# Performance work log

Measured on AMD Instinct MI355X. Metric: run time of the kernel, lower is better.

## Reference

```python
import jax, jax.numpy as jnp
import numpy as np

B, S, D = 4, 2048, 2048
H, G, HD = 16, 4, 128  # n_heads, kv groups, head_dim
EPS = 1e-6


def setup_inputs() -> dict:
    key = jax.random.key(0)
    ks = jax.random.split(key, 8)
    x = jax.random.normal(ks[0], (B, S, D), dtype=jnp.float32)
    # causal mask, True = attend (already 'inverted' for SDPA semantics)
    mask = jnp.tril(jnp.ones((S, S), dtype=bool))
    # RoPE tables: (S, HD), rotate-half convention with duplicated freqs
    inv_freq = 1.0 / (10000.0 ** (np.arange(0, HD, 2, dtype=np.float32) / HD))
    ang = np.arange(S, dtype=np.float32)[:, None] * inv_freq[None, :]  # (S, HD/2)
    ang = np.concatenate([ang, ang], axis=-1)  # (S, HD)
    cos = jnp.asarray(np.cos(ang))
    sin = jnp.asarray(np.sin(ang))
    s = 0.02
    wq = jax.random.normal(ks[1], (D, H * HD), dtype=jnp.float32) * s
    wk = jax.random.normal(ks[2], (D, G * HD), dtype=jnp.float32) * s
    wv = jax.random.normal(ks[3], (D, G * HD), dtype=jnp.float32) * s
    wg = jax.random.normal(ks[4], (D, H * HD), dtype=jnp.float32) * s
    wo = jax.random.normal(ks[5], (H * HD, D), dtype=jnp.float32) * s
    q_scale = jax.random.normal(ks[6], (HD,), dtype=jnp.float32) * 0.01  # zero-centered
    k_scale = jax.random.normal(ks[7], (HD,), dtype=jnp.float32) * 0.01
    return dict(x=x, mask=mask, cos=cos, sin=sin, wq=wq, wk=wk, wv=wv,
                wg=wg, wo=wo, q_scale=q_scale, k_scale=k_scale)


def _zc_rmsnorm(x, scale):
    # zero-centered RMSNorm in fp32: x * rsqrt(mean(x^2)+eps) * (1+scale)
    xf = x.astype(jnp.float32)
    rms = jax.lax.rsqrt(jnp.mean(xf * xf, axis=-1, keepdims=True) + EPS)
    return (xf * rms * (1.0 + scale)).astype(x.dtype)


def _rope(x, cos, sin):
    # x: (b, h, s, hd); cos/sin: (s, hd)
    hd = x.shape[-1]
    x1, x2 = x[..., : hd // 2], x[..., hd // 2 :]
    rot = jnp.concatenate([-x2, x1], axis=-1)
    return x * cos[None, None] + rot * sin[None, None]


def reference(x, mask, cos, sin, wq, wk, wv, wg, wo, q_scale, k_scale):
    b, s, d = x.shape
    q = (x @ wq).reshape(b, s, H, HD).transpose(0, 2, 1, 3)   # (b,H,s,hd)
    k = (x @ wk).reshape(b, s, G, HD).transpose(0, 2, 1, 3)   # (b,G,s,hd)
    v = (x @ wv).reshape(b, s, G, HD).transpose(0, 2, 1, 3)
    gate = jax.nn.sigmoid(x @ wg)                              # (b,s,H*HD)

    q = _rope(_zc_rmsnorm(q, q_scale), cos, sin)
    k = _rope(_zc_rmsnorm(k, k_scale), cos, sin)

    rep = H // G
    k = jnp.repeat(k, rep, axis=1)   # (b,H,s,hd)
    v = jnpep = jnp.repeat(v, rep, axis=1) if False else jnp.repeat(v, rep, axis=1)

    scores = jnp.einsum('bhqd,bhkd->bhqk', q, k) / jnp.sqrt(jnp.float32(HD))
    scores = jnp.where(mask[None, None, :s, :s], scores, jnp.float32(-1e30))
    attn = jax.nn.softmax(scores, axis=-1)
    ctx = jnp.einsum('bhqk,bhkd->bhqd', attn, v)               # (b,H,s,hd)
    ctx = ctx.transpose(0, 2, 1, 3).reshape(b, s, H * HD)
    return (ctx * gate) @ wo
```

## Files before the change

### kernel.cpp

```cpp
#include <hip/hip_runtime.h>

typedef __bf16 bf16;
typedef __attribute__((ext_vector_type(8))) __bf16 bf16x8;
typedef __attribute__((ext_vector_type(4))) float f32x4;

constexpr int Bb = 4, S = 2048, Dd = 2048, H = 16, G = 4, HD = 128;
constexpr float L2E = 1.4426950408889634f;

__device__ inline f32x4 mfma16(bf16x8 a, bf16x8 b, f32x4 c) {
  return __builtin_amdgcn_mfma_f32_16x16x32_bf16(a, b, c, 0, 0, 0);
}

__device__ inline void gl_lds16(const void* g, void* l) {
  __builtin_amdgcn_global_load_lds(
      (const __attribute__((address_space(1))) void*)g,
      (__attribute__((address_space(3))) void*)l, 16, 0, 0);
}

__global__ __launch_bounds__(256) void k_f32_to_bf16(
    const float* __restrict__ in, bf16* __restrict__ out, int n8) {
  int i = blockIdx.x * 256 + threadIdx.x;
  if (i >= n8) return;
  const float4* p = (const float4*)(in + (long long)i * 8);
  float4 a = p[0], b = p[1];
  bf16x8 v;
  v[0] = (bf16)a.x; v[1] = (bf16)a.y; v[2] = (bf16)a.z; v[3] = (bf16)a.w;
  v[4] = (bf16)b.x; v[5] = (bf16)b.y; v[6] = (bf16)b.z; v[7] = (bf16)b.w;
  *(bf16x8*)(out + (long long)i * 8) = v;
}

template <typename InT>
__global__ __launch_bounds__(256) void k_transpose_bf16(
    const InT* __restrict__ in, long long s1, int nb2, long long s2, int ldin,
    bf16* __restrict__ out, long long obatch, int ldout, int R, int C) {
  __shared__ float tile[32][33];
  int z = blockIdx.z;
  const InT* ip = in + (long long)(z / nb2) * s1 + (long long)(z % nb2) * s2;
  bf16* op = out + (long long)z * obatch;
  int c0 = blockIdx.x * 32, r0 = blockIdx.y * 32;
  int tx = threadIdx.x, ty = threadIdx.y;
#pragma unroll
  for (int i = 0; i < 4; ++i) {
    int r = r0 + ty + i * 8, c = c0 + tx;
    tile[ty + i * 8][tx] = (r < R && c < C) ? (float)ip[(long long)r * ldin + c] : 0.f;
  }
  __syncthreads();
#pragma unroll
  for (int i = 0; i < 4; ++i) {
    int c = c0 + ty + i * 8, r = r0 + tx;
    if (c < C && r < R) op[(long long)c * ldout + r] = (bf16)tile[tx][ty + i * 8];
  }
}

template <typename CT>
__global__ __launch_bounds__(512, 2) void k_gemm256(
    const bf16* __restrict__ A, int lda, const bf16* __restrict__ Bt, int ldb,
    CT* __restrict__ C, int ldc, int M, int N, int K) {
  __shared__ bf16 ldsbuf[65536];
  char* lds2 = (char*)ldsbuf;
  const int tid = threadIdx.x;
  const int w = tid >> 6, lane = tid & 63;
  const int l16 = lane & 15, lh = lane >> 4;
  const int wr = w >> 2, wc = w & 3;
  const int nbn = N >> 8;
  const int cpx = gridDim.x >> 3;
  const int swz = (blockIdx.x & 7) * cpx + (blockIdx.x >> 3);
  const int bm = swz / nbn, bn = swz % nbn;
  const int m0 = bm << 8, n0 = bn << 8;

  const int lrow = lane >> 3;
  const int lcol = ((lane & 7) ^ lrow) * 8;
  const int arb = wr * 128 + wc * 16;
  const int xg = wc >> 1, sg = wr * 2 + (wc & 1);
  const int brb = xg * 128 + (sg >> 1) * 64 + (sg & 1) * 16;
  const bf16* aS0 = A + (long long)(m0 + arb + lrow) * lda + lcol;
  const bf16* aS1 = A + (long long)(m0 + arb + 8 + lrow) * lda + lcol;
  const bf16* bS0 = Bt + (long long)(n0 + brb + lrow) * ldb + lcol;
  const bf16* bS1 = Bt + (long long)(n0 + brb + 8 + lrow) * ldb + lcol;

  auto stageA = [&](int buf, int k0, int hi) {
    gl_lds16(aS0 + (long long)hi * 64 * lda + k0,
             lds2 + buf * 65536 + (arb + hi * 64) * 128);
    gl_lds16(aS1 + (long long)hi * 64 * lda + k0,
             lds2 + buf * 65536 + (arb + hi * 64 + 8) * 128);
  };
  auto stageB = [&](int buf, int k0, int hi) {
    gl_lds16(bS0 + (long long)hi * 32 * ldb + k0,
             lds2 + buf * 65536 + 32768 + (brb + hi * 32) * 128);
    gl_lds16(bS1 + (long long)hi * 32 * ldb + k0,
             lds2 + buf * 65536 + 32768 + (brb + hi * 32 + 8) * 128);
  };

  f32x4 acc[8][4] = {};
  const int NT = K >> 6;

  stageA(0, 0, 0);
  stageB(0, 0, 0);
  stageB(0, 0, 1);
  stageA(0, 0, 1);
  asm volatile("s_waitcnt vmcnt(4)" ::: "memory");
  __builtin_amdgcn_s_barrier();

  const int swzc = (l16 & 7) << 4;
  for (int t = 0; t < NT; ++t) {
    const int buf = t & 1, nb = buf ^ 1;
    const int kn = (t + 1) << 6;
    const bool more = (t + 1 < NT);
    const char* La = lds2 + buf * 65536;
    const char* Lb = La + 32768;
    bf16x8 af[4][2], bn0[2][2], bn1[2][2];
    if (more) stageA(nb, kn, 0);
#pragma unroll
    for (int m = 0; m < 4; ++m)
#pragma unroll
      for (int ks = 0; ks < 2; ++ks)
        af[m][ks] = *(const bf16x8*)(La + (wr * 128 + m * 16 + l16) * 128 +
                                     ((ks * 64 + lh * 16) ^ swzc));
#pragma unroll
    for (int n = 0; n < 2; ++n)
#pragma unroll
      for (int ks = 0; ks < 2; ++ks)
        bn0[n][ks] = *(const bf16x8*)(Lb + (wc * 64 + n * 16 + l16) * 128 +
                                      ((ks * 64 + lh * 16) ^ swzc));
    __builtin_amdgcn_s_barrier();
    asm volatile("s_waitcnt lgkmcnt(0)" ::: "memory");
    __builtin_amdgcn_sched_barrier(0);
    __builtin_amdgcn_s_setprio(1);
#pragma unroll
    for (int m = 0; m < 4; ++m)
#pragma unroll
      for (int n = 0; n < 2; ++n)
#pragma unroll
        for (int ks = 0; ks < 2; ++ks)
          acc[m][n] = mfma16(af[m][ks], bn0[n][ks], acc[m][n]);
    __builtin_amdgcn_s_setprio(0);
    asm volatile("s_waitcnt vmcnt(4)" ::: "memory");
    __builtin_amdgcn_s_barrier();
    if (more) stageB(nb, kn, 0);
#pragma unroll
    for (int n = 0; n < 2; ++n)
#pragma unroll
      for (int ks = 0; ks < 2; ++ks)
        bn1[n][ks] = *(const bf16x8*)(Lb + (wc * 64 + 32 + n * 16 + l16) * 128 +
                                      ((ks * 64 + lh * 16) ^ swzc));
    __builtin_amdgcn_s_barrier();
    asm volatile("s_waitcnt lgkmcnt(0)" ::: "memory");
    __builtin_amdgcn_sched_barrier(0);
    __builtin_amdgcn_s_setprio(1);
#pragma unroll
    for (int m = 0; m < 4; ++m)
#pragma unroll
      for (int n = 0; n < 2; ++n)
#pragma unroll
        for (int ks = 0; ks < 2; ++ks)
          acc[m][2 + n] = mfma16(af[m][ks], bn1[n][ks], acc[m][2 + n]);
    __builtin_amdgcn_s_setprio(0);
    asm volatile("s_waitcnt vmcnt(4)" ::: "memory");
    __builtin_amdgcn_s_barrier();
    if (more) stageB(nb, kn, 1);
#pragma unroll
    for (int m = 0; m < 4; ++m)
#pragma unroll
      for (int ks = 0; ks < 2; ++ks)
        af[m][ks] = *(const bf16x8*)(La + (wr * 128 + 64 + m * 16 + l16) * 128 +
                                     ((ks * 64 + lh * 16) ^ swzc));
    __builtin_amdgcn_s_barrier();
    asm volatile("s_waitcnt lgkmcnt(0)" ::: "memory");
    __builtin_amdgcn_sched_barrier(0);
    __builtin_amdgcn_s_setprio(1);
#pragma unroll
    for (int m = 0; m < 4; ++m)
#pragma unroll
      for (int n = 0; n < 2; ++n)
#pragma unroll
        for (int ks = 0; ks < 2; ++ks)
          acc[4 + m][2 + n] = mfma16(af[m][ks], bn1[n][ks], acc[4 + m][2 + n]);
    __builtin_amdgcn_s_setprio(0);
    __builtin_amdgcn_s_barrier();
    if (more) stageA(nb, kn, 1);
    __builtin_amdgcn_s_barrier();
    __builtin_amdgcn_s_setprio(1);
#pragma unroll
    for (int m = 0; m < 4; ++m)
#pragma unroll
      for (int n = 0; n < 2; ++n)
#pragma unroll
        for (int ks = 0; ks < 2; ++ks)
          acc[4 + m][n] = mfma16(af[m][ks], bn0[n][ks], acc[4 + m][n]);
    __builtin_amdgcn_s_setprio(0);
    asm volatile("s_waitcnt vmcnt(4)" ::: "memory");
    __builtin_amdgcn_s_barrier();
  }

#pragma unroll
  for (int m = 0; m < 8; ++m)
#pragma unroll
    for (int n = 0; n < 4; ++n)
#pragma unroll
      for (int r = 0; r < 4; ++r)
        C[(long long)(m0 + wr * 128 + m * 16 + lh * 4 + r) * ldc + n0 + wc * 64 +
          n * 16 + l16] = (CT)acc[m][n][r];
}

__global__ __launch_bounds__(256) void k_rms_rope(
    const bf16* __restrict__ in, int ldin, int nh, const float* __restrict__ scale,
    const float* __restrict__ cosT, const float* __restrict__ sinT,
    bf16* __restrict__ out, float oscale, int nwaves) {
  int wid = (blockIdx.x * 256 + threadIdx.x) >> 6;
  if (wid >= nwaves) return;
  int lane = threadIdx.x & 63;
  int h = wid % nh;
  int bs = wid / nh;
  int s = bs % S;
  int b = bs / S;
  const bf16* ip = in + (long long)bs * ldin + h * HD;
  float x1 = (float)ip[lane], x2 = (float)ip[lane + 64];
  float ss = x1 * x1 + x2 * x2;
#pragma unroll
  for (int m = 1; m < 64; m <<= 1) ss += __shfl_xor(ss, m);
  float rms = rsqrtf(ss * (1.f / 128.f) + 1e-6f);
  float n1 = x1 * rms * (1.f + scale[lane]);
  float n2 = x2 * rms * (1.f + scale[lane + 64]);
  float o1 = (n1 * cosT[s * 128 + lane] - n2 * sinT[s * 128 + lane]) * oscale;
  float o2 = (n2 * cosT[s * 128 + lane + 64] + n1 * sinT[s * 128 + lane + 64]) * oscale;
  bf16* op = out + (((long long)b * nh + h) * S + s) * HD;
  op[lane] = (bf16)o1;
  op[lane + 64] = (bf16)o2;
}

__global__ __launch_bounds__(256) void k_sigmoid(bf16* __restrict__ p, int ld,
                                                 int cols8, int n) {
  int i = blockIdx.x * 256 + threadIdx.x;
  if (i >= n) return;
  int row = i / cols8, c = (i % cols8) * 8;
  bf16x8* q = (bf16x8*)(p + (long long)row * ld + c);
  bf16x8 v = *q;
#pragma unroll
  for (int j = 0; j < 8; ++j) {
    float f = (float)v[j];
    v[j] = (bf16)(1.f / (1.f + exp2f(-f * L2E)));
  }
  *q = v;
}

__global__ __launch_bounds__(512, 2) void k_flash2(
    const bf16* __restrict__ Q, const bf16* __restrict__ Kb,
    const bf16* __restrict__ Vt, const bf16* __restrict__ gate, int ldg,
    bf16* __restrict__ outc, int ldo) {
  __shared__ bf16 Ks[2][64 * 128];
  __shared__ bf16 Vs[2][128 * 64];
  __shared__ bf16 Ps[8][32 * 72];
  const int tid = threadIdx.x, w = tid >> 6, lane = tid & 63;
  const int l16 = lane & 15, lh = lane >> 4;
  const int bh = blockIdx.x & 63;
  const int qi = blockIdx.x >> 6;
  const int qc = 7 - qi;
  const int h = bh & 15, b = bh >> 4, g = h >> 2;
  const int qbase = qc * 256;
  const int q0w = qbase + w * 32;
  const bf16* qp = Q + (((long long)b * H + h) * S + q0w) * HD;
  const bf16* kp = Kb + ((long long)b * G + g) * S * HD;
  const bf16* vp = Vt + ((long long)b * G + g) * (long long)HD * S;

  bf16x8 aq[2][4];
#pragma unroll
  for (int m = 0; m < 2; ++m)
#pragma unroll
    for (int ks = 0; ks < 4; ++ks)
      aq[m][ks] = *(const bf16x8*)(qp + (long long)(m * 16 + l16) * HD + ks * 32 + lh * 8);

  f32x4 acc[2][8] = {};
  float mrow[2][4], lrow[2][4];
#pragma unroll
  for (int m = 0; m < 2; ++m)
#pragma unroll
    for (int r = 0; r < 4; ++r) { mrow[m][r] = -1e30f; lrow[m][r] = 0.f; }

  const int ntiles = qc * 4 + 4;

  auto stage = [&](int bi, int t) {
    const int kv0 = t << 6;
#pragma unroll
    for (int i = 0; i < 2; ++i) {
      int c = w * 128 + i * 64 + lane;
      int row = c >> 4;
      int cb = ((c & 15) << 4) ^ ((row & 7) << 4);
      gl_lds16(kp + (long long)(kv0 + row) * HD + (cb >> 1),
               (char*)Ks[bi] + (w * 128 + i * 64) * 16);
      int rowv = c >> 3;
      int cbv = ((c & 7) << 4) ^ ((rowv & 7) << 4);
      gl_lds16(vp + (long long)rowv * S + kv0 + (cbv >> 1),
               (char*)Vs[bi] + (w * 128 + i * 64) * 16);
    }
  };

  stage(0, 0);
  __syncthreads();

  for (int t = 0; t < ntiles; ++t) {
    const int buf = t & 1;
    if (t + 1 < ntiles) stage(buf ^ 1, t + 1);
    const int kv0 = t << 6;
    if (kv0 <= q0w + 31) {
      f32x4 s[2][4] = {};
#pragma unroll
      for (int ks = 0; ks < 4; ++ks)
#pragma unroll
        for (int n = 0; n < 4; ++n) {
          int row = n * 16 + l16;
          int off = row * 256 + ((ks * 64 + lh * 16) ^ ((row & 7) << 4));
          bf16x8 kb = *(const bf16x8*)((const char*)Ks[buf] + off);
#pragma unroll
          for (int m = 0; m < 2; ++m) s[m][n] = mfma16(aq[m][ks], kb, s[m][n]);
        }
      if (kv0 + 63 > q0w) {
#pragma unroll
        for (int m = 0; m < 2; ++m)
#pragma unroll
          for (int n = 0; n < 4; ++n)
#pragma unroll
            for (int r = 0; r < 4; ++r) {
              int col = kv0 + n * 16 + l16;
              int rowg = q0w + m * 16 + lh * 4 + r;
              if (col > rowg) s[m][n][r] = -1e30f;
            }
      }
      float pm[2][4];
#pragma unroll
      for (int m = 0; m < 2; ++m)
#pragma unroll
        for (int r = 0; r < 4; ++r)
          pm[m][r] = fmaxf(fmaxf(s[m][0][r], s[m][1][r]), fmaxf(s[m][2][r], s[m][3][r]));
#pragma unroll
      for (int st = 1; st < 16; st <<= 1)
#pragma unroll
        for (int m = 0; m < 2; ++m)
#pragma unroll
          for (int r = 0; r < 4; ++r) pm[m][r] = fmaxf(pm[m][r], __shfl_xor(pm[m][r], st));
      float resc[2][4];
#pragma unroll
      for (int m = 0; m < 2; ++m)
#pragma unroll
        for (int r = 0; r < 4; ++r) {
          float mn = fmaxf(mrow[m][r], pm[m][r]);
          resc[m][r] = exp2f(mrow[m][r] - mn);
          mrow[m][r] = mn;
        }
#pragma unroll
      for (int m = 0; m < 2; ++m)
#pragma unroll
        for (int n = 0; n < 4; ++n) {
#pragma unroll
          for (int r = 0; r < 4; ++r) {
            float p = exp2f(s[m][n][r] - mrow[m][r]);
            s[m][n][r] = p;
            Ps[w][(m * 16 + lh * 4 + r) * 72 + n * 16 + l16] = (bf16)p;
          }
        }
#pragma unroll
      for (int m = 0; m < 2; ++m)
#pragma unroll
        for (int r = 0; r < 4; ++r)
          lrow[m][r] = lrow[m][r] * resc[m][r] +
                       (s[m][0][r] + s[m][1][r] + s[m][2][r] + s[m][3][r]);
#pragma unroll
      for (int m = 0; m < 2; ++m)
#pragma unroll
        for (int dt = 0; dt < 8; ++dt)
#pragma unroll
          for (int r = 0; r < 4; ++r) acc[m][dt][r] *= resc[m][r];
      bf16x8 pa[2][2];
#pragma unroll
      for (int m = 0; m < 2; ++m)
#pragma unroll
        for (int kf = 0; kf < 2; ++kf)
          pa[m][kf] = *(const bf16x8*)((const char*)&Ps[w][0] +
                                       (m * 16 + l16) * 144 + kf * 64 + lh * 16);
#pragma unroll
      for (int dt = 0; dt < 8; ++dt) {
        int d = dt * 16 + l16;
#pragma unroll
        for (int kf = 0; kf < 2; ++kf) {
          int off = d * 128 + ((kf * 64 + lh * 16) ^ ((d & 7) << 4));
          bf16x8 vb = *(const bf16x8*)((const char*)Vs[buf] + off);
#pragma unroll
          for (int m = 0; m < 2; ++m) acc[m][dt] = mfma16(pa[m][kf], vb, acc[m][dt]);
        }
      }
    }
    __syncthreads();
  }

#pragma unroll
  for (int st = 1; st < 16; st <<= 1)
#pragma unroll
    for (int m = 0; m < 2; ++m)
#pragma unroll
      for (int r = 0; r < 4; ++r) lrow[m][r] += __shfl_xor(lrow[m][r], st);
  float inv[2][4];
#pragma unroll
  for (int m = 0; m < 2; ++m)
#pragma unroll
    for (int r = 0; r < 4; ++r) inv[m][r] = 1.f / lrow[m][r];
#pragma unroll
  for (int m = 0; m < 2; ++m)
#pragma unroll
    for (int dt = 0; dt < 8; ++dt)
#pragma unroll
      for (int r = 0; r < 4; ++r) {
        int rowg = q0w + m * 16 + lh * 4 + r;
        long long row = (long long)b * S + rowg;
        int col = h * HD + dt * 16 + l16;
        float gv = (float)gate[row * ldg + col];
        outc[row * ldo + col] = (bf16)(acc[m][dt][r] * inv[m][r] * gv);
      }
}

extern "C" void kernel_launch(void* const* d_in, const int* in_sizes, int n_in,
                              void* d_out, int out_size, void* d_ws, size_t ws_size,
                              hipStream_t stream) {
  const float* x = (const float*)d_in[0];
  const float* cosT = (const float*)d_in[2];
  const float* sinT = (const float*)d_in[3];
  const float* wq = (const float*)d_in[4];
  const float* wk = (const float*)d_in[5];
  const float* wv = (const float*)d_in[6];
  const float* wg = (const float*)d_in[7];
  const float* wo = (const float*)d_in[8];
  const float* qs = (const float*)d_in[9];
  const float* ksc = (const float*)d_in[10];
  float* out = (float*)d_out;
  char* ws = (char*)d_ws;

  if (ws_size < 146800640) return;
  bf16* xb = (bf16*)(ws);
  bf16* wcat = (bf16*)(ws + 33554432);
  bf16* woT = (bf16*)(ws + 54525952);
  bf16* C1 = (bf16*)(ws + 62914560);
  bf16* qbuf = xb;
  bf16* kbuf = wcat;
  bf16* vtbuf = wcat + 4194304;
  bf16* gatep = C1 + 3072;
  bf16* ctxg = C1;

  dim3 tb(32, 8);
  k_f32_to_bf16<<<8192, 256, 0, stream>>>(x, xb, Bb * S * Dd / 8);
  k_transpose_bf16<float><<<dim3(64, 64, 1), tb, 0, stream>>>(
      wq, 0, 1, 0, 2048, wcat, 0, 2048, 2048, 2048);
  k_transpose_bf16<float><<<dim3(16, 64, 1), tb, 0, stream>>>(
      wk, 0, 1, 0, 512, wcat + 2048 * 2048, 0, 2048, 2048, 512);
  k_transpose_bf16<float><<<dim3(16, 64, 1), tb, 0, stream>>>(
      wv, 0, 1, 0, 512, wcat + 2560 * 2048, 0, 2048, 2048, 512);
  k_transpose_bf16<float><<<dim3(64, 64, 1), tb, 0, stream>>>(
      wg, 0, 1, 0, 2048, wcat + 3072 * 2048, 0, 2048, 2048, 2048);
  k_transpose_bf16<float><<<dim3(64, 64, 1), tb, 0, stream>>>(
      wo, 0, 1, 0, 2048, woT, 0, 2048, 2048, 2048);
  k_gemm256<bf16><<<32 * 20, 512, 0, stream>>>(xb, 2048, wcat, 2048, C1, 5120,
                                               8192, 5120, 2048);
  k_rms_rope<<<32768, 256, 0, stream>>>(C1, 5120, 16, qs, cosT, sinT, qbuf,
                                        0.12751879523209308f, 131072);
  k_rms_rope<<<8192, 256, 0, stream>>>(C1 + 2048, 5120, 4, ksc, cosT, sinT, kbuf,
                                       1.0f, 32768);
  k_transpose_bf16<bf16><<<dim3(4, 64, 16), tb, 0, stream>>>(
      C1 + 2560, (long long)2048 * 5120, 4, 128, 5120, vtbuf,
      (long long)128 * 2048, 2048, 2048, 128);
  k_sigmoid<<<8192, 256, 0, stream>>>(gatep, 5120, 256, 2097152);
  k_flash2<<<512, 512, 0, stream>>>(qbuf, kbuf, vtbuf, gatep, 5120, ctxg, 5120);
  k_gemm256<float><<<32 * 8, 512, 0, stream>>>(ctxg, 5120, woT, 2048, out, 2048,
                                               8192, 2048, 2048);
}
```

Baseline: 514.0 us.

## Software-pipeline LDS fragment reads across GEMM sub-phases and drop extra barriers

Restructures the GEMM main loop so LDS fragment reads for the next quarter-tile are issued while the current MFMA block executes. This removes the lgkmcnt(0) wait and the extra barrier in front of each MFMA group. It also prefetches the first A half of tile t+2 into the buffer just consumed, and guards staging with a k<K check. The gain is better overlap of LDS and global loads with MFMAs. The cost is more live fragment registers and a more delicate vmcnt/barrier ordering that could race or cause spills.

```diff
diff --git a/kernel.cpp b/kernel.cpp
--- a/kernel.cpp
+++ b/kernel.cpp
@@ -79,51 +79,59 @@
   const bf16* bS1 = Bt + (long long)(n0 + brb + 8 + lrow) * ldb + lcol;
 
   auto stageA = [&](int buf, int k0, int hi) {
+    if (k0 >= K) return;
     gl_lds16(aS0 + (long long)hi * 64 * lda + k0,
              lds2 + buf * 65536 + (arb + hi * 64) * 128);
     gl_lds16(aS1 + (long long)hi * 64 * lda + k0,
              lds2 + buf * 65536 + (arb + hi * 64 + 8) * 128);
   };
   auto stageB = [&](int buf, int k0, int hi) {
+    if (k0 >= K) return;
     gl_lds16(bS0 + (long long)hi * 32 * ldb + k0,
              lds2 + buf * 65536 + 32768 + (brb + hi * 32) * 128);
     gl_lds16(bS1 + (long long)hi * 32 * ldb + k0,
              lds2 + buf * 65536 + 32768 + (brb + hi * 32 + 8) * 128);
   };
 
+  const int swzc = (l16 & 7) << 4;
+  auto rdA = [&](bf16x8 (&dst)[4][2], const char* L, int mh) {
+#pragma unroll
+    for (int m = 0; m < 4; ++m)
+#pragma unroll
+      for (int ks = 0; ks < 2; ++ks)
+        dst[m][ks] = *(const bf16x8*)(L + (wr * 128 + mh * 64 + m * 16 + l16) * 128 +
+                                      ((ks * 64 + lh * 16) ^ swzc));
+  };
+  auto rdB = [&](bf16x8 (&dst)[2][2], const char* L, int nh) {
+#pragma unroll
+    for (int n = 0; n < 2; ++n)
+#pragma unroll
+      for (int ks = 0; ks < 2; ++ks)
+        dst[n][ks] = *(const bf16x8*)(L + 32768 + (wc * 64 + nh * 32 + n * 16 + l16) * 128 +
+                                      ((ks * 64 + lh * 16) ^ swzc));
+  };
+
   f32x4 acc[8][4] = {};
+  bf16x8 aflo[4][2], afhi[4][2], bn0[2][2], bn1[2][2], bn0b[2][2];
   const int NT = K >> 6;
 
   stageA(0, 0, 0);
   stageB(0, 0, 0);
   stageB(0, 0, 1);
   stageA(0, 0, 1);
+  stageA(1, 64, 0);
   asm volatile("s_waitcnt vmcnt(4)" ::: "memory");
   __builtin_amdgcn_s_barrier();
-
-  const int swzc = (l16 & 7) << 4;
+  rdA(aflo, lds2, 0);
+  rdB(bn0, lds2, 0);
+
   for (int t = 0; t < NT; ++t) {
-    const int buf = t & 1, nb = buf ^ 1;
-    const int kn = (t + 1) << 6;
-    const bool more = (t + 1 < NT);
-    const char* La = lds2 + buf * 65536;
-    const char* Lb = La + 32768;
-    bf16x8 af[4][2], bn0[2][2], bn1[2][2];
-    if (more) stageA(nb, kn, 0);
-#pragma unroll
-    for (int m = 0; m < 4; ++m)
-#pragma unroll
-      for (int ks = 0; ks < 2; ++ks)
-        af[m][ks] = *(const bf16x8*)(La + (wr * 128 + m * 16 + l16) * 128 +
-                                     ((ks * 64 + lh * 16) ^ swzc));
-#pragma unroll
-    for (int n = 0; n < 2; ++n)
-#pragma unroll
-      for (int ks = 0; ks < 2; ++ks)
-        bn0[n][ks] = *(const bf16x8*)(Lb + (wc * 64 + n * 16 + l16) * 128 +
-                                      ((ks * 64 + lh * 16) ^ swzc));
-    __builtin_amdgcn_s_barrier();
-    asm volatile("s_waitcnt lgkmcnt(0)" ::: "memory");
+    const int buf = t & 1;
+    const char* L = lds2 + buf * 65536;
+    const char* Ln = lds2 + (buf ^ 1) * 65536;
+    const int k1 = (t + 1) << 6;
+    rdB(bn1, L, 1);
+    stageB(buf ^ 1, k1, 0);
     __builtin_amdgcn_sched_barrier(0);
     __builtin_amdgcn_s_setprio(1);
 #pragma unroll
@@ -132,19 +140,12 @@
       for (int n = 0; n < 2; ++n)
 #pragma unroll
         for (int ks = 0; ks < 2; ++ks)
-          acc[m][n] = mfma16(af[m][ks], bn0[n][ks], acc[m][n]);
+          acc[m][n] = mfma16(aflo[m][ks], bn0[n][ks], acc[m][n]);
     __builtin_amdgcn_s_setprio(0);
     asm volatile("s_waitcnt vmcnt(4)" ::: "memory");
     __builtin_amdgcn_s_barrier();
-    if (more) stageB(nb, kn, 0);
-#pragma unroll
-    for (int n = 0; n < 2; ++n)
-#pragma unroll
-      for (int ks = 0; ks < 2; ++ks)
-        bn1[n][ks] = *(const bf16x8*)(Lb + (wc * 64 + 32 + n * 16 + l16) * 128 +
-                                      ((ks * 64 + lh * 16) ^ swzc));
-    __builtin_amdgcn_s_barrier();
-    asm volatile("s_waitcnt lgkmcnt(0)" ::: "memory");
+    rdA(afhi, L, 1);
+    stageB(buf ^ 1, k1, 1);
     __builtin_amdgcn_sched_barrier(0);
     __builtin_amdgcn_s_setprio(1);
 #pragma unroll
@@ -153,19 +154,12 @@
       for (int n = 0; n < 2; ++n)
 #pragma unroll
         for (int ks = 0; ks < 2; ++ks)
-          acc[m][2 + n] = mfma16(af[m][ks], bn1[n][ks], acc[m][2 + n]);
+          acc[m][2 + n] = mfma16(aflo[m][ks], bn1[n][ks], acc[m][2 + n]);
     __builtin_amdgcn_s_setprio(0);
     asm volatile("s_waitcnt vmcnt(4)" ::: "memory");
     __builtin_amdgcn_s_barrier();
-    if (more) stageB(nb, kn, 1);
-#pragma unroll
-    for (int m = 0; m < 4; ++m)
-#pragma unroll
-      for (int ks = 0; ks < 2; ++ks)
-        af[m][ks] = *(const bf16x8*)(La + (wr * 128 + 64 + m * 16 + l16) * 128 +
-                                     ((ks * 64 + lh * 16) ^ swzc));
-    __builtin_amdgcn_s_barrier();
-    asm volatile("s_waitcnt lgkmcnt(0)" ::: "memory");
+    rdB(bn0b, L, 0);
+    stageA(buf ^ 1, k1, 1);
     __builtin_amdgcn_sched_barrier(0);
     __builtin_amdgcn_s_setprio(1);
 #pragma unroll
@@ -174,11 +168,16 @@
       for (int n = 0; n < 2; ++n)
 #pragma unroll
         for (int ks = 0; ks < 2; ++ks)
-          acc[4 + m][2 + n] = mfma16(af[m][ks], bn1[n][ks], acc[4 + m][2 + n]);
+          acc[4 + m][2 + n] = mfma16(afhi[m][ks], bn1[n][ks], acc[4 + m][2 + n]);
     __builtin_amdgcn_s_setprio(0);
+    asm volatile("s_waitcnt vmcnt(4)" ::: "memory");
     __builtin_amdgcn_s_barrier();
-    if (more) stageA(nb, kn, 1);
-    __builtin_amdgcn_s_barrier();
+    if (t + 1 < NT) {
+      rdA(aflo, Ln, 0);
+      rdB(bn0, Ln, 0);
+    }
+    stageA(buf, (t + 2) << 6, 0);
+    __builtin_amdgcn_sched_barrier(0);
     __builtin_amdgcn_s_setprio(1);
 #pragma unroll
     for (int m = 0; m < 4; ++m)
@@ -186,7 +185,7 @@
       for (int n = 0; n < 2; ++n)
 #pragma unroll
         for (int ks = 0; ks < 2; ++ks)
-          acc[4 + m][n] = mfma16(af[m][ks], bn0[n][ks], acc[4 + m][n]);
+          acc[4 + m][n] = mfma16(afhi[m][ks], bn0b[n][ks], acc[4 + m][n]);
     __builtin_amdgcn_s_setprio(0);
     asm volatile("s_waitcnt vmcnt(4)" ::: "memory");
     __builtin_amdgcn_s_barrier();
```

Measured after the change: 708.6 us. +37.8%, slower.

## Split K/V staging, lazy softmax rescale, and swizzle P tile in flash attention

Applied to the files above, without the earlier changes.

The flash-attention kernel now single-buffers V and issues its load at the start of each tile, while K for the next tile is double-buffered. Raw s_barrier calls with explicit vmcnt waits replace __syncthreads, so the V load overlaps the QK^T and softmax work. The online softmax skips the cross-lane max reduction and accumulator rescale when every lane's new local max stays within 8 (log2 units) of the running max. The P scratch tile drops its padding and uses an XOR swizzle. This trades extra barriers and a weaker max bound (which risks overflow if the threshold is violated) for less reduction work and lower LDS use.

```diff
diff --git a/kernel.cpp b/kernel.cpp
--- a/kernel.cpp
+++ b/kernel.cpp
@@ -243,13 +243,13 @@
   *q = v;
 }
 
-__global__ __launch_bounds__(512, 2) void k_flash2(
+__global__ __launch_bounds__(512, 2) void k_flash3(
     const bf16* __restrict__ Q, const bf16* __restrict__ Kb,
     const bf16* __restrict__ Vt, const bf16* __restrict__ gate, int ldg,
     bf16* __restrict__ outc, int ldo) {
   __shared__ bf16 Ks[2][64 * 128];
-  __shared__ bf16 Vs[2][128 * 64];
-  __shared__ bf16 Ps[8][32 * 72];
+  __shared__ bf16 Vs[128 * 64];
+  __shared__ bf16 Ps[8][32 * 64];
   const int tid = threadIdx.x, w = tid >> 6, lane = tid & 63;
   const int l16 = lane & 15, lh = lane >> 4;
   const int bh = blockIdx.x & 63;
@@ -278,7 +278,7 @@
 
   const int ntiles = qc * 4 + 4;
 
-  auto stage = [&](int bi, int t) {
+  auto stageK = [&](int bi, int t) {
     const int kv0 = t << 6;
 #pragma unroll
     for (int i = 0; i < 2; ++i) {
@@ -287,21 +287,32 @@
       int cb = ((c & 15) << 4) ^ ((row & 7) << 4);
       gl_lds16(kp + (long long)(kv0 + row) * HD + (cb >> 1),
                (char*)Ks[bi] + (w * 128 + i * 64) * 16);
+    }
+  };
+  auto stageV = [&](int t) {
+    const int kv0 = t << 6;
+#pragma unroll
+    for (int i = 0; i < 2; ++i) {
+      int c = w * 128 + i * 64 + lane;
       int rowv = c >> 3;
       int cbv = ((c & 7) << 4) ^ ((rowv & 7) << 4);
       gl_lds16(vp + (long long)rowv * S + kv0 + (cbv >> 1),
-               (char*)Vs[bi] + (w * 128 + i * 64) * 16);
+               (char*)Vs + (w * 128 + i * 64) * 16);
     }
   };
 
-  stage(0, 0);
-  __syncthreads();
+  stageK(0, 0);
+  asm volatile("s_waitcnt vmcnt(0)" ::: "memory");
+  __builtin_amdgcn_s_barrier();
+  asm volatile("" ::: "memory");
 
   for (int t = 0; t < ntiles; ++t) {
     const int buf = t & 1;
-    if (t + 1 < ntiles) stage(buf ^ 1, t + 1);
     const int kv0 = t << 6;
-    if (kv0 <= q0w + 31) {
+    const bool active = (kv0 <= q0w + 31);
+    stageV(t);
+    if (t + 1 < ntiles) stageK(buf ^ 1, t + 1);
+    if (active) {
       f32x4 s[2][4] = {};
 #pragma unroll
       for (int ks = 0; ks < 4; ++ks)
@@ -325,70 +336,80 @@
               if (col > rowg) s[m][n][r] = -1e30f;
             }
       }
-      float pm[2][4];
+      float lm[2][4];
+      bool okl = true;
 #pragma unroll
       for (int m = 0; m < 2; ++m)
 #pragma unroll
-        for (int r = 0; r < 4; ++r)
-          pm[m][r] = fmaxf(fmaxf(s[m][0][r], s[m][1][r]), fmaxf(s[m][2][r], s[m][3][r]));
-#pragma unroll
-      for (int st = 1; st < 16; st <<= 1)
+        for (int r = 0; r < 4; ++r) {
+          lm[m][r] = fmaxf(fmaxf(s[m][0][r], s[m][1][r]), fmaxf(s[m][2][r], s[m][3][r]));
+          okl = okl && (lm[m][r] <= mrow[m][r] + 8.f);
+        }
+      if (!__all(okl)) {
+#pragma unroll
+        for (int st = 1; st < 16; st <<= 1)
+#pragma unroll
+          for (int m = 0; m < 2; ++m)
+#pragma unroll
+            for (int r = 0; r < 4; ++r) lm[m][r] = fmaxf(lm[m][r], __shfl_xor(lm[m][r], st));
 #pragma unroll
         for (int m = 0; m < 2; ++m)
 #pragma unroll
-          for (int r = 0; r < 4; ++r) pm[m][r] = fmaxf(pm[m][r], __shfl_xor(pm[m][r], st));
-      float resc[2][4];
+          for (int r = 0; r < 4; ++r) {
+            float mn = fmaxf(mrow[m][r], lm[m][r]);
+            float resc = exp2f(mrow[m][r] - mn);
+            mrow[m][r] = mn;
+            lrow[m][r] *= resc;
+#pragma unroll
+            for (int dt = 0; dt < 8; ++dt) acc[m][dt][r] *= resc;
+          }
+      }
 #pragma unroll
       for (int m = 0; m < 2; ++m)
 #pragma unroll
-        for (int r = 0; r < 4; ++r) {
-          float mn = fmaxf(mrow[m][r], pm[m][r]);
-          resc[m][r] = exp2f(mrow[m][r] - mn);
-          mrow[m][r] = mn;
-        }
-#pragma unroll
-      for (int m = 0; m < 2; ++m)
-#pragma unroll
-        for (int n = 0; n < 4; ++n) {
+        for (int n = 0; n < 4; ++n)
 #pragma unroll
           for (int r = 0; r < 4; ++r) {
             float p = exp2f(s[m][n][r] - mrow[m][r]);
             s[m][n][r] = p;
-            Ps[w][(m * 16 + lh * 4 + r) * 72 + n * 16 + l16] = (bf16)p;
+            int row = m * 16 + lh * 4 + r;
+            *(bf16*)((char*)Ps[w] + row * 128 +
+                     ((n * 32 + l16 * 2) ^ ((row & 7) << 4))) = (bf16)p;
           }
+#pragma unroll
+      for (int m = 0; m < 2; ++m)
+#pragma unroll
+        for (int r = 0; r < 4; ++r)
+          lrow[m][r] += s[m][0][r] + s[m][1][r] + s[m][2][r] + s[m][3][r];
+    }
+    asm volatile("s_waitcnt vmcnt(2)" ::: "memory");
+    __builtin_amdgcn_s_barrier();
+    asm volatile("" ::: "memory");
+    if (active) {
+      bf16x8 pa[2][2];
+#pragma unroll
+      for (int m = 0; m < 2; ++m)
+#pragma unroll
+        for (int kf = 0; kf < 2; ++kf) {
+          int row = m * 16 + l16;
+          pa[m][kf] = *(const bf16x8*)((const char*)Ps[w] + row * 128 +
+                                       ((kf * 64 + lh * 16) ^ ((row & 7) << 4)));
         }
-#pragma unroll
-      for (int m = 0; m < 2; ++m)
-#pragma unroll
-        for (int r = 0; r < 4; ++r)
-          lrow[m][r] = lrow[m][r] * resc[m][r] +
-                       (s[m][0][r] + s[m][1][r] + s[m][2][r] + s[m][3][r]);
-#pragma unroll
-      for (int m = 0; m < 2; ++m)
-#pragma unroll
-        for (int dt = 0; dt < 8; ++dt)
-#pragma unroll
-          for (int r = 0; r < 4; ++r) acc[m][dt][r] *= resc[m][r];
-      bf16x8 pa[2][2];
-#pragma unroll
-      for (int m = 0; m < 2; ++m)
-#pragma unroll
-        for (int kf = 0; kf < 2; ++kf)
-          pa[m][kf] = *(const bf16x8*)((const char*)&Ps[w][0] +
-                                       (m * 16 + l16) * 144 + kf * 64 + lh * 16);
 #pragma unroll
       for (int dt = 0; dt < 8; ++dt) {
         int d = dt * 16 + l16;
 #pragma unroll
         for (int kf = 0; kf < 2; ++kf) {
           int off = d * 128 + ((kf * 64 + lh * 16) ^ ((d & 7) << 4));
-          bf16x8 vb = *(const bf16x8*)((const char*)Vs[buf] + off);
+          bf16x8 vb = *(const bf16x8*)((const char*)Vs + off);
 #pragma unroll
           for (int m = 0; m < 2; ++m) acc[m][dt] = mfma16(pa[m][kf], vb, acc[m][dt]);
         }
       }
     }
-    __syncthreads();
+    asm volatile("s_waitcnt vmcnt(0)" ::: "memory");
+    __builtin_amdgcn_s_barrier();
+    asm volatile("" ::: "memory");
   }
 
 #pragma unroll
@@ -465,7 +486,7 @@
       C1 + 2560, (long long)2048 * 5120, 4, 128, 5120, vtbuf,
       (long long)128 * 2048, 2048, 2048, 128);
   k_sigmoid<<<8192, 256, 0, stream>>>(gatep, 5120, 256, 2097152);
-  k_flash2<<<512, 512, 0, stream>>>(qbuf, kbuf, vtbuf, gatep, 5120, ctxg, 5120);
+  k_flash3<<<512, 512, 0, stream>>>(qbuf, kbuf, vtbuf, gatep, 5120, ctxg, 5120);
   k_gemm256<float><<<32 * 8, 512, 0, stream>>>(ctxg, 5120, woT, 2048, out, 2048,
                                                8192, 2048, 2048);
 }
```

Measured after the change: 478.9 us. 6.8% less time.
